# Optimization experiments

Measured on AMD Instinct MI355X. Metric: run time of the kernel, lower is better.

Reference implementation:

```python
import jax, jax.numpy as jnp
import numpy as np
import math

D_MODEL = 512
N_HEADS = 2
B, S = 2, 1024
THRESHOLD = 0.5  # kwargs default 'sparsity_threshold'


def setup_inputs() -> dict:
    key = jax.random.key(0)
    ks = jax.random.split(key, 10)
    D, H = D_MODEL, D_MODEL // 4
    std = 0.02
    return {
        "x": jax.random.normal(ks[0], (B, S, D), jnp.float32),
        "Wq": jax.random.normal(ks[1], (D, D), jnp.float32) * std,
        "Wk": jax.random.normal(ks[2], (D, D), jnp.float32) * std,
        "Wv": jax.random.normal(ks[3], (D, D), jnp.float32) * std,
        "Wo": jax.random.normal(ks[4], (D, D), jnp.float32) * std,
        "bo": jnp.zeros((D,), jnp.float32),
        "W1": jax.random.normal(ks[5], (D, H), jnp.float32) * std,
        "b1": jnp.zeros((H,), jnp.float32),
        "W2": jax.random.normal(ks[6], (H, 1), jnp.float32) * std,
        "b2": jnp.zeros((1,), jnp.float32),
    }


def reference(x, Wq, Wk, Wv, Wo, bo, W1, b1, W2, b2):
    Bsz, Seq, D = x.shape
    Hn = N_HEADS
    dh = D // Hn

    def split_heads(t):
        return t.reshape(Bsz, Seq, Hn, dh).transpose(0, 2, 1, 3)  # [B,H,S,dh]

    q = split_heads(x @ Wq)
    k = split_heads(x @ Wk)
    v = split_heads(x @ Wv)

    scores = jnp.einsum("bhid,bhjd->bhij", q, k) / math.sqrt(dh)  # [B,H,S,S]

    # head-mean features for the pairwise sparsity predictor (n_heads==2 => 2*dh == D)
    q_mean = q.mean(axis=1)  # [B,S,dh]
    k_mean = k.mean(axis=1)  # [B,S,dh]
    # Linear1 of cat([q_mean_i, k_mean_j]) splits into two halves of W1
    a = q_mean @ W1[:dh]   # [B,S,Dh4]
    c = k_mean @ W1[dh:]   # [B,S,Dh4]
    hidden = jax.nn.relu(a[:, :, None, :] + c[:, None, :, :] + b1)  # [B,S,S,Dh4]
    connection_probs = jax.nn.sigmoid(jnp.squeeze(hidden @ W2, -1) + b2[0])  # [B,S,S]

    mask = connection_probs > THRESHOLD  # [B,S,S]
    scores = jnp.where(mask[:, None, :, :], scores, jnp.float32(-1e9))
    attn = jax.nn.softmax(scores, axis=-1)  # dropout inactive in eval

    out = jnp.einsum("bhij,bhjd->bhid", attn, v)  # [B,H,S,dh]
    out = out.transpose(0, 2, 1, 3).reshape(Bsz, Seq, D)
    out = out @ Wo + bo
    return out
```

## Files before the change

### kernel.cpp

```cpp
#include <hip/hip_runtime.h>


typedef unsigned short u16t;
typedef __bf16 bf16x8 __attribute__((ext_vector_type(8)));
typedef float f32x4 __attribute__((ext_vector_type(4)));

#define B_SZ 2
#define S_SZ 1024
#define D_SZ 512
#define DH 256
#define HH 128

static __device__ __forceinline__ u16t f2b(float f) {
    unsigned int u = __builtin_bit_cast(unsigned int, f);
    u += 0x7FFFu + ((u >> 16) & 1u);
    return (u16t)(u >> 16);
}

static __device__ __forceinline__ f32x4 mfma16(bf16x8 a, bf16x8 b, f32x4 c) {
    return __builtin_amdgcn_mfma_f32_16x16x32_bf16(a, b, c, 0, 0, 0);
}

static __device__ __forceinline__ void gload16(const void* g, void* l) {
    __builtin_amdgcn_global_load_lds(
        (const __attribute__((address_space(1))) void*)g,
        (__attribute__((address_space(3))) void*)l, 16, 0, 0);
}

__global__ __launch_bounds__(256) void k_prep(
    const float* __restrict__ x,
    const float* __restrict__ Wq, const float* __restrict__ Wk,
    const float* __restrict__ Wv, const float* __restrict__ Wo,
    const float* __restrict__ W1,
    u16t* __restrict__ xb, u16t* __restrict__ WT, float* __restrict__ Beff)
{
    __shared__ float smf[1088];
    int bidx = blockIdx.x;
    int t = threadIdx.x;
    if (bidx < 1024) {
        int idx = (bidx * 256 + t) * 4;
        float4 v = *(const float4*)(x + idx);
        u16t* o = xb + idx;
        o[0] = f2b(v.x); o[1] = f2b(v.y); o[2] = f2b(v.z); o[3] = f2b(v.w);
    } else if (bidx < 2048) {
        int t2 = bidx - 1024;
        int z = t2 >> 8, rem = t2 & 255;
        int n0 = (rem & 15) * 32, k0 = (rem >> 4) * 32;
        const float* W = z == 0 ? Wq : z == 1 ? Wk : z == 2 ? Wv : Wo;
        u16t* WTz = WT + (size_t)z * D_SZ * D_SZ;
        float (*tile)[33] = (float(*)[33])smf;
        int r = t >> 3, c4 = (t & 7) * 4;
        float4 v = *(const float4*)(W + (size_t)(k0 + r) * D_SZ + n0 + c4);
        tile[r][c4] = v.x; tile[r][c4 + 1] = v.y; tile[r][c4 + 2] = v.z; tile[r][c4 + 3] = v.w;
        __syncthreads();
        u16t o[4];
        o[0] = f2b(tile[c4][r]); o[1] = f2b(tile[c4 + 1][r]);
        o[2] = f2b(tile[c4 + 2][r]); o[3] = f2b(tile[c4 + 3][r]);
        *(ushort4*)(WTz + (size_t)(n0 + r) * D_SZ + k0 + c4) = *(ushort4*)o;
    } else {
        int k = bidx - 2048;
        float* wm0 = smf;
        float* wm1 = smf + 256;
        const float* wrq = Wq + (size_t)k * D_SZ;
        const float* wrk = Wk + (size_t)k * D_SZ;
        wm0[t & 255] = 0.5f * (wrq[t & 255] + wrq[(t & 255) + DH]);
        wm1[t & 255] = 0.5f * (wrk[t & 255] + wrk[(t & 255) + DH]);
        __syncthreads();
        int half = t >> 7, hcol = t & 127;
        const float* wm = half ? wm1 : wm0;
        const float* W1h = W1 + (half ? (size_t)DH * HH : 0);
        float s = 0.f;
        for (int d = 0; d < 256; ++d) s += wm[d] * W1h[(size_t)d * HH + hcol];
        Beff[(size_t)k * 256 + half * 128 + hcol] = s;
    }
}

template<int MF, int NF>
static __device__ __forceinline__ void gemm_db(
    const u16t* __restrict__ A, int lda, const u16t* __restrict__ B, int ldb,
    int K, int tid, u16t* Als, u16t* Bls, f32x4 acc[MF][NF])
{
    const int w = tid >> 6, lane = tid & 63;
    const int lr = lane & 15, kg = lane >> 4;
    const int srow = lane >> 3;
    const int scol = ((lane & 7) ^ srow) * 8;
    const int ABUF = MF * 4096;
    const int BBUF = NF * 1024;
    auto stage = [&](int bb, int k0) {
#pragma unroll
        for (int q = 0; q < MF * 2; ++q) {
            int ci = w * (MF * 2) + q;
            gload16(A + (size_t)(ci * 8 + srow) * lda + k0 + scol,
                    Als + bb * ABUF + ci * 512);
        }
#pragma unroll
        for (int q = 0; q < NF / 2; ++q) {
            int cj = w * (NF / 2) + q;
            gload16(B + (size_t)(cj * 8 + srow) * ldb + k0 + scol,
                    Bls + bb * BBUF + cj * 512);
        }
    };
    stage(0, 0);
    __syncthreads();
    const int nt = K / 64;
    for (int t = 0; t < nt; ++t) {
        int cur = t & 1;
        if (t + 1 < nt) stage(cur ^ 1, (t + 1) * 64);
        const u16t* Ab = Als + cur * ABUF;
        const u16t* Bb = Bls + cur * BBUF;
#pragma unroll
        for (int kk = 0; kk < 2; ++kk) {
            bf16x8 af[MF], bfr[NF];
#pragma unroll
            for (int fi = 0; fi < MF; ++fi) {
                int r = w * (MF * 16) + fi * 16 + lr;
                af[fi] = *(const bf16x8*)(&Ab[r * 64 + (((kk * 4 + kg) ^ (r & 7)) << 3)]);
            }
#pragma unroll
            for (int fj = 0; fj < NF; ++fj) {
                int r = fj * 16 + lr;
                bfr[fj] = *(const bf16x8*)(&Bb[r * 64 + (((kk * 4 + kg) ^ (r & 7)) << 3)]);
            }
#pragma unroll
            for (int fi = 0; fi < MF; ++fi)
#pragma unroll
                for (int fj = 0; fj < NF; ++fj)
                    acc[fi][fj] = mfma16(af[fi], bfr[fj], acc[fi][fj]);
        }
        __syncthreads();
    }
}


__global__ __launch_bounds__(256) void k_qkvac(
    const u16t* __restrict__ xb, const u16t* __restrict__ WT,
    const float* __restrict__ x, const float* __restrict__ Beff,
    const float* __restrict__ b1,
    u16t* __restrict__ qb, u16t* __restrict__ kb, u16t* __restrict__ vT,
    float* __restrict__ a, float* __restrict__ cc)
{
    __shared__ __align__(16) char sm[49152];
    int bid = blockIdx.x;
    int t = threadIdx.x;
    if (bid < 384) {
        u16t* Als = (u16t*)sm;
        u16t* Bls = (u16t*)(sm + 32768);
        int z = bid / 128, rem = bid & 127;
        int m0 = (rem >> 3) * 128, n0 = (rem & 7) * 64;
        const u16t* A = xb + (size_t)m0 * D_SZ;
        const u16t* Bt = WT + (size_t)z * D_SZ * D_SZ + (size_t)n0 * D_SZ;
        f32x4 acc[2][4] = {};
        gemm_db<2, 4>(A, D_SZ, Bt, D_SZ, D_SZ, t, Als, Bls, acc);
        int w = t >> 6, lane = t & 63, lr = lane & 15, kg = lane >> 4;
        if (z < 2) {
            u16t (*vls)[68] = (u16t(*)[68])sm;
            float scale = z == 0 ? 0.0625f : 1.0f;
#pragma unroll
            for (int fi = 0; fi < 2; ++fi)
#pragma unroll
                for (int fj = 0; fj < 4; ++fj)
#pragma unroll
                    for (int rr = 0; rr < 4; ++rr)
                        vls[w * 32 + fi * 16 + kg * 4 + rr][fj * 16 + lr]
                            = f2b(acc[fi][fj][rr] * scale);
            __syncthreads();
            u16t* dst = z == 0 ? qb : kb;
            int c8 = (t & 7) * 8, r0 = t >> 3;
#pragma unroll
            for (int p = 0; p < 4; ++p) {
                int r = r0 + p * 32;
                *(uint4*)(dst + (size_t)(m0 + r) * D_SZ + n0 + c8) = *(const uint4*)(&vls[r][c8]);
            }
        } else {
            u16t (*vls)[136] = (u16t(*)[136])sm;
#pragma unroll
            for (int fi = 0; fi < 2; ++fi)
#pragma unroll
                for (int fj = 0; fj < 4; ++fj)
#pragma unroll
                    for (int rr = 0; rr < 4; ++rr)
                        vls[fj * 16 + lr][w * 32 + fi * 16 + kg * 4 + rr] = f2b(acc[fi][fj][rr]);
            __syncthreads();
            int b = m0 >> 10, s0 = m0 & 1023;
            int cr = t >> 2, seg = t & 3;
            const u16t* srcp = &vls[cr][seg * 32];
            u16t* dstp = vT + (((size_t)(b * D_SZ + n0 + cr)) << 10) + s0 + seg * 32;
#pragma unroll
            for (int qq = 0; qq < 4; ++qq)
                *(uint4*)(dstp + qq * 8) = *(const uint4*)(srcp + qq * 8);
        }
    } else {
        float (*xs)[68] = (float(*)[68])sm;
        float (*bsT)[68] = (float(*)[68])(sm + 17408);
        int t2 = bid - 384;
        int r0 = (t2 & 31) * 64, n0 = (t2 >> 5) * 32;
        int ti = t >> 4, tj = t & 15;
        float acc[4][2] = {};
        for (int k0 = 0; k0 < 512; k0 += 64) {
            if (k0) __syncthreads();
#pragma unroll
            for (int p = 0; p < 4; ++p) {
                int idx = t + p * 256;
                int r = idx >> 4, c4 = (idx & 15) * 4;
                *(float4*)&xs[r][c4] = *(const float4*)(x + (size_t)(r0 + r) * D_SZ + k0 + c4);
            }
#pragma unroll
            for (int p = 0; p < 2; ++p) {
                int idx = t + p * 256;
                int k = idx >> 3, n4 = (idx & 7) * 4;
                float4 v = *(const float4*)(Beff + (size_t)(k0 + k) * 256 + n0 + n4);
                bsT[n4][k] = v.x; bsT[n4 + 1][k] = v.y; bsT[n4 + 2][k] = v.z; bsT[n4 + 3][k] = v.w;
            }
            __syncthreads();
#pragma unroll
            for (int kk = 0; kk < 16; ++kk) {
                float4 xv[4], bv[2];
#pragma unroll
                for (int ri = 0; ri < 4; ++ri) xv[ri] = *(const float4*)&xs[ti + 16 * ri][kk * 4];
#pragma unroll
                for (int rj = 0; rj < 2; ++rj) bv[rj] = *(const float4*)&bsT[tj + 16 * rj][kk * 4];
#pragma unroll
                for (int ri = 0; ri < 4; ++ri)
#pragma unroll
                    for (int rj = 0; rj < 2; ++rj)
                        acc[ri][rj] += xv[ri].x * bv[rj].x + xv[ri].y * bv[rj].y
                                     + xv[ri].z * bv[rj].z + xv[ri].w * bv[rj].w;
            }
        }
        bool isA = n0 < 128;
#pragma unroll
        for (int rj = 0; rj < 2; ++rj) {
            int col = n0 + tj + 16 * rj;
            float badd = isA ? b1[col] : 0.f;
#pragma unroll
            for (int ri = 0; ri < 4; ++ri) {
                int row = r0 + ti + 16 * ri;
                if (isA) a[(size_t)row * HH + col] = acc[ri][rj] + badd;
                else     cc[(size_t)row * HH + (col - 128)] = acc[ri][rj];
            }
        }
    }
}

__global__ __launch_bounds__(256) void k_scores(
    const u16t* __restrict__ qb, const u16t* __restrict__ kb,
    const float* __restrict__ a, const float* __restrict__ c,
    const float* __restrict__ W2, const float* __restrict__ b2,
    u16t* __restrict__ P, float* __restrict__ lpart)
{
    __shared__ __align__(16) char sm[55296];
    float (*at)[132] = (float(*)[132])sm;
    float (*ct)[132] = (float(*)[132])(sm + 33792);
    unsigned char (*msk)[64] = (unsigned char(*)[64])(sm + 50688);
    float* w2s = (float*)(sm + 54784);
    int b = blockIdx.z, mt = blockIdx.y, jb = blockIdx.x;
    int m0 = mt * 64, j0 = jb * 64;
    int t = threadIdx.x;
    if (t < 128) w2s[t] = W2[t];
#pragma unroll
    for (int p = 0; p < 8; ++p) {
        int idx = t + p * 256;
        int r = idx >> 5, c4 = (idx & 31) * 4;
        *(float4*)&at[r][c4] = *(const float4*)(a + ((size_t)(b * S_SZ + m0 + r)) * HH + c4);
    }
    float fb2 = b2[0];
    int ti = t >> 4, tj = t & 15;
#pragma unroll
    for (int jh = 0; jh < 2; ++jh) {
        __syncthreads();
#pragma unroll
        for (int p = 0; p < 4; ++p) {
            int idx = t + p * 256;
            int r = idx >> 5, c4 = (idx & 31) * 4;
            *(float4*)&ct[r][c4] =
                *(const float4*)(c + ((size_t)(b * S_SZ + j0 + jh * 32 + r)) * HH + c4);
        }
        __syncthreads();
        float accm[4][2];
#pragma unroll
        for (int ri = 0; ri < 4; ++ri)
#pragma unroll
            for (int rj = 0; rj < 2; ++rj) accm[ri][rj] = fb2;
#pragma unroll 2
        for (int h4 = 0; h4 < 32; ++h4) {
            float4 wv = ((const float4*)w2s)[h4];
            float4 av[4], cv[2];
#pragma unroll
            for (int ri = 0; ri < 4; ++ri) av[ri] = *(const float4*)&at[ti + 16 * ri][h4 * 4];
#pragma unroll
            for (int rj = 0; rj < 2; ++rj) cv[rj] = *(const float4*)&ct[tj + 16 * rj][h4 * 4];
#pragma unroll
            for (int ri = 0; ri < 4; ++ri)
#pragma unroll
                for (int rj = 0; rj < 2; ++rj) {
                    accm[ri][rj] += fmaxf(av[ri].x + cv[rj].x, 0.f) * wv.x;
                    accm[ri][rj] += fmaxf(av[ri].y + cv[rj].y, 0.f) * wv.y;
                    accm[ri][rj] += fmaxf(av[ri].z + cv[rj].z, 0.f) * wv.z;
                    accm[ri][rj] += fmaxf(av[ri].w + cv[rj].w, 0.f) * wv.w;
                }
        }
#pragma unroll
        for (int ri = 0; ri < 4; ++ri)
#pragma unroll
            for (int rj = 0; rj < 2; ++rj)
                msk[ti + 16 * ri][jh * 32 + tj + 16 * rj] = accm[ri][rj] > 0.f ? 1 : 0;
    }
    __syncthreads();
    u16t* Als = (u16t*)sm;
    u16t* Bls = (u16t*)(sm + 16384);
    const u16t* A = qb + (size_t)(b * S_SZ + m0) * D_SZ;
    const u16t* B = kb + (size_t)(b * S_SZ + j0) * D_SZ;
    const int w = t >> 6, lane = t & 63, lr = lane & 15, kg = lane >> 4;
    const int srow = lane >> 3;
    const int scol = ((lane & 7) ^ srow) * 8;
    auto stage = [&](int bb, int k0) {
#pragma unroll
        for (int q = 0; q < 2; ++q) {
            int ci = w * 2 + q;
            gload16(A + (size_t)(ci * 8 + srow) * D_SZ + k0 + scol, Als + bb * 4096 + ci * 512);
            gload16(B + (size_t)(ci * 8 + srow) * D_SZ + k0 + scol, Bls + bb * 4096 + ci * 512);
        }
    };
    f32x4 acc0[4] = {}, acc1[4] = {};
    stage(0, 0);
    __syncthreads();
#pragma unroll
    for (int t8 = 0; t8 < 8; ++t8) {
        int cur = t8 & 1;
        if (t8 < 7) stage(cur ^ 1, (t8 + 1) * 64);
        const u16t* Ab = Als + cur * 4096;
        const u16t* Bb = Bls + cur * 4096;
#pragma unroll
        for (int kk = 0; kk < 2; ++kk) {
            int ra = w * 16 + lr;
            bf16x8 af = *(const bf16x8*)(&Ab[ra * 64 + (((kk * 4 + kg) ^ (ra & 7)) << 3)]);
            bf16x8 bfr[4];
#pragma unroll
            for (int fj = 0; fj < 4; ++fj) {
                int rb = fj * 16 + lr;
                bfr[fj] = *(const bf16x8*)(&Bb[rb * 64 + (((kk * 4 + kg) ^ (rb & 7)) << 3)]);
            }
            if (t8 < 4) {
#pragma unroll
                for (int fj = 0; fj < 4; ++fj) acc0[fj] = mfma16(af, bfr[fj], acc0[fj]);
            } else {
#pragma unroll
                for (int fj = 0; fj < 4; ++fj) acc1[fj] = mfma16(af, bfr[fj], acc1[fj]);
            }
        }
        __syncthreads();
    }
    u16t (*vls)[68] = (u16t(*)[68])sm;
#pragma unroll
    for (int h = 0; h < 2; ++h) {
#pragma unroll
        for (int rr = 0; rr < 4; ++rr) {
            int il = w * 16 + kg * 4 + rr;
            float rs = 0.f;
#pragma unroll
            for (int fj = 0; fj < 4; ++fj) {
                int jl = fj * 16 + lr;
                float s = h ? acc1[fj][rr] : acc0[fj][rr];
                float e = msk[il][jl] ? __expf(s) : 0.f;
                if (h) acc1[fj][rr] = e; else acc0[fj][rr] = e;
                rs += e;
            }
            rs += __shfl_xor(rs, 1); rs += __shfl_xor(rs, 2);
            rs += __shfl_xor(rs, 4); rs += __shfl_xor(rs, 8);
            if (lr == 0)
                lpart[((size_t)(jb * 4 + b * 2 + h) << 10) + m0 + il] = rs;
        }
#pragma unroll
        for (int fj = 0; fj < 4; ++fj)
#pragma unroll
            for (int rr = 0; rr < 4; ++rr)
                vls[w * 16 + kg * 4 + rr][fj * 16 + lr]
                    = f2b(h ? acc1[fj][rr] : acc0[fj][rr]);
        __syncthreads();
        int r = t >> 2, c16 = (t & 3) * 16;
        u16t* dstp = P + ((size_t)(b * 2 + h) << 20) + ((size_t)(m0 + r) << 10) + j0 + c16;
        *(uint4*)dstp = *(const uint4*)(&vls[r][c16]);
        *(uint4*)(dstp + 8) = *(const uint4*)(&vls[r][c16 + 8]);
        __syncthreads();
    }
}

__global__ __launch_bounds__(256) void k_pv(
    const u16t* __restrict__ P, const u16t* __restrict__ vT,
    const float* __restrict__ lpart, u16t* __restrict__ ao)
{
    __shared__ __align__(16) u16t sm[12288];
    __shared__ float invl[64];
    u16t* Als = sm;
    u16t* Bls = sm + 8192;
    int bh = blockIdx.z, b = bh >> 1, h = bh & 1;
    int m0 = blockIdx.y * 64, n0 = blockIdx.x * 32;
    int t = threadIdx.x;
    if (t < 64) {
        float l = 0.f;
        for (int jb = 0; jb < 16; ++jb)
            l += lpart[((size_t)(jb * 4 + bh) << 10) + m0 + t];
        invl[t] = l > 0.f ? 1.0f / l : 0.f;
    }
    const u16t* A = P + ((size_t)bh << 20) + (size_t)m0 * S_SZ;
    const u16t* Bt = vT + ((size_t)(b * D_SZ + h * DH + n0)) * S_SZ;
    f32x4 acc[1][2] = {};
    gemm_db<1, 2>(A, S_SZ, Bt, S_SZ, S_SZ, t, Als, Bls, acc);
    int w = t >> 6, lane = t & 63, lr = lane & 15, kg = lane >> 4;
    u16t (*ols)[40] = (u16t(*)[40])sm;
#pragma unroll
    for (int fj = 0; fj < 2; ++fj)
#pragma unroll
        for (int rr = 0; rr < 4; ++rr) {
            int rl = w * 16 + kg * 4 + rr;
            ols[rl][fj * 16 + lr] = f2b(acc[0][fj][rr] * invl[rl]);
        }
    __syncthreads();
    int r = t >> 2, c8 = (t & 3) * 8;
    *(uint4*)(ao + ((size_t)(b * S_SZ + m0 + r)) * D_SZ + h * DH + n0 + c8)
        = *(const uint4*)(&ols[r][c8]);
}

__global__ __launch_bounds__(256) void k_out(
    const u16t* __restrict__ ao, const u16t* __restrict__ WoT,
    const float* __restrict__ bo, float* __restrict__ out)
{
    __shared__ __align__(16) u16t sm[12288];
    u16t* Als = sm;
    u16t* Bls = sm + 8192;
    int m0 = blockIdx.y * 64, n0 = blockIdx.x * 32;
    const u16t* A = ao + (size_t)m0 * D_SZ;
    const u16t* Bt = WoT + (size_t)n0 * D_SZ;
    f32x4 acc[1][2] = {};
    gemm_db<1, 2>(A, D_SZ, Bt, D_SZ, D_SZ, threadIdx.x, Als, Bls, acc);
    int w = threadIdx.x >> 6, lane = threadIdx.x & 63, lr = lane & 15, kg = lane >> 4;
    float (*ols)[36] = (float(*)[36])sm;
#pragma unroll
    for (int fj = 0; fj < 2; ++fj)
#pragma unroll
        for (int rr = 0; rr < 4; ++rr) {
            int rl = w * 16 + kg * 4 + rr;
            ols[rl][fj * 16 + lr] = acc[0][fj][rr] + bo[n0 + fj * 16 + lr];
        }
    __syncthreads();
    int r0 = threadIdx.x >> 3, c4 = (threadIdx.x & 7) * 4;
#pragma unroll
    for (int p = 0; p < 2; ++p) {
        int r = r0 + p * 32;
        *(float4*)(out + (size_t)(m0 + r) * D_SZ + n0 + c4) = *(const float4*)(&ols[r][c4]);
    }
}

extern "C" void kernel_launch(void* const* d_in, const int* in_sizes, int n_in,
                              void* d_out, int out_size, void* d_ws, size_t ws_size,
                              hipStream_t stream)
{
    const float* x  = (const float*)d_in[0];
    const float* Wq = (const float*)d_in[1];
    const float* Wk = (const float*)d_in[2];
    const float* Wv = (const float*)d_in[3];
    const float* Wo = (const float*)d_in[4];
    const float* bo = (const float*)d_in[5];
    const float* W1 = (const float*)d_in[6];
    const float* b1 = (const float*)d_in[7];
    const float* W2 = (const float*)d_in[8];
    const float* b2 = (const float*)d_in[9];
    float* out = (float*)d_out;

    char* ws = (char*)d_ws;
    size_t off = 0;
    auto carve = [&](size_t bytes) { void* p = ws + off; off += (bytes + 255) & ~(size_t)255; return p; };
    u16t* xb   = (u16t*)carve((size_t)2048 * 512 * 2);
    u16t* WT   = (u16t*)carve((size_t)4 * 512 * 512 * 2);
    u16t* qb   = (u16t*)carve((size_t)2048 * 512 * 2);
    u16t* kb   = (u16t*)carve((size_t)2048 * 512 * 2);
    u16t* vT   = (u16t*)carve((size_t)2 * 512 * 1024 * 2);
    float* Beff = (float*)carve((size_t)512 * 256 * 4);
    float* a   = (float*)carve((size_t)2048 * 128 * 4);
    float* c   = (float*)carve((size_t)2048 * 128 * 4);
    u16t* P    = (u16t*)carve((size_t)4 * 1024 * 1024 * 2);
    float* lpart = (float*)carve((size_t)16 * 4 * 1024 * 4);
    u16t* ao   = (u16t*)carve((size_t)2048 * 512 * 2);
    (void)ws_size;

    k_prep<<<dim3(2560), dim3(256), 0, stream>>>(x, Wq, Wk, Wv, Wo, W1, xb, WT, Beff);
    k_qkvac<<<dim3(640), dim3(256), 0, stream>>>(xb, WT, x, Beff, b1, qb, kb, vT, a, c);
    k_scores<<<dim3(16, 16, 2), dim3(256), 0, stream>>>(qb, kb, a, c, W2, b2, P, lpart);
    k_pv<<<dim3(8, 16, 4), dim3(256), 0, stream>>>(P, vT, lpart, ao);
    k_out<<<dim3(16, 32), dim3(256), 0, stream>>>(ao, WT + (size_t)3 * 512 * 512, bo, out);
}
```

Measured before the change: 100.3 us.

## Halve k_scores row tile to 32 and remap waves to column strips

Halves the query-row tile of the scores/mask kernel from 64 to 32 rows, doubling the grid to 1024 blocks and shrinking shared memory so more blocks fit per CU. Each wave now owns a 16-column strip of keys instead of a 16-row strip, so row sums are reduced across waves through a small shared buffer before being written. The aim is more parallelism and occupancy on the many-CU GPU, at the cost of reloading the key tile and c-vectors twice as often and an extra barrier for the cross-wave sum.

New measurement: 99.78 us (median of 2 runs). Within noise of the previous version (-0.5%).

```diff
diff --git a/kernel.cpp b/kernel.cpp
--- a/kernel.cpp
+++ b/kernel.cpp
@@ -248,23 +248,24 @@
     const float* __restrict__ W2, const float* __restrict__ b2,
     u16t* __restrict__ P, float* __restrict__ lpart)
 {
-    __shared__ __align__(16) char sm[55296];
+    __shared__ __align__(16) char sm[36864];
     float (*at)[132] = (float(*)[132])sm;
-    float (*ct)[132] = (float(*)[132])(sm + 33792);
-    unsigned char (*msk)[64] = (unsigned char(*)[64])(sm + 50688);
-    float* w2s = (float*)(sm + 54784);
+    float (*ct)[132] = (float(*)[132])(sm + 16896);
+    unsigned char (*msk)[64] = (unsigned char(*)[64])(sm + 33792);
+    float* w2s  = (float*)(sm + 35840);
+    float* lsum = (float*)(sm + 36352);
     int b = blockIdx.z, mt = blockIdx.y, jb = blockIdx.x;
-    int m0 = mt * 64, j0 = jb * 64;
+    int m0 = mt * 32, j0 = jb * 64;
     int t = threadIdx.x;
     if (t < 128) w2s[t] = W2[t];
-#pragma unroll
-    for (int p = 0; p < 8; ++p) {
+    float fb2 = b2[0];
+    int ti = t >> 4, tj = t & 15;
+#pragma unroll
+    for (int p = 0; p < 4; ++p) {
         int idx = t + p * 256;
         int r = idx >> 5, c4 = (idx & 31) * 4;
         *(float4*)&at[r][c4] = *(const float4*)(a + ((size_t)(b * S_SZ + m0 + r)) * HH + c4);
     }
-    float fb2 = b2[0];
-    int ti = t >> 4, tj = t & 15;
 #pragma unroll
     for (int jh = 0; jh < 2; ++jh) {
         __syncthreads();
@@ -276,21 +277,21 @@
                 *(const float4*)(c + ((size_t)(b * S_SZ + j0 + jh * 32 + r)) * HH + c4);
         }
         __syncthreads();
-        float accm[4][2];
-#pragma unroll
-        for (int ri = 0; ri < 4; ++ri)
+        float accm[2][2];
+#pragma unroll
+        for (int ri = 0; ri < 2; ++ri)
 #pragma unroll
             for (int rj = 0; rj < 2; ++rj) accm[ri][rj] = fb2;
 #pragma unroll 2
         for (int h4 = 0; h4 < 32; ++h4) {
             float4 wv = ((const float4*)w2s)[h4];
-            float4 av[4], cv[2];
-#pragma unroll
-            for (int ri = 0; ri < 4; ++ri) av[ri] = *(const float4*)&at[ti + 16 * ri][h4 * 4];
+            float4 av[2], cv[2];
+#pragma unroll
+            for (int ri = 0; ri < 2; ++ri) av[ri] = *(const float4*)&at[ti + 16 * ri][h4 * 4];
 #pragma unroll
             for (int rj = 0; rj < 2; ++rj) cv[rj] = *(const float4*)&ct[tj + 16 * rj][h4 * 4];
 #pragma unroll
-            for (int ri = 0; ri < 4; ++ri)
+            for (int ri = 0; ri < 2; ++ri)
 #pragma unroll
                 for (int rj = 0; rj < 2; ++rj) {
                     accm[ri][rj] += fmaxf(av[ri].x + cv[rj].x, 0.f) * wv.x;
@@ -300,52 +301,52 @@
                 }
         }
 #pragma unroll
-        for (int ri = 0; ri < 4; ++ri)
+        for (int ri = 0; ri < 2; ++ri)
 #pragma unroll
             for (int rj = 0; rj < 2; ++rj)
                 msk[ti + 16 * ri][jh * 32 + tj + 16 * rj] = accm[ri][rj] > 0.f ? 1 : 0;
     }
     __syncthreads();
     u16t* Als = (u16t*)sm;
-    u16t* Bls = (u16t*)(sm + 16384);
+    u16t* Bls = (u16t*)(sm + 8192);
     const u16t* A = qb + (size_t)(b * S_SZ + m0) * D_SZ;
     const u16t* B = kb + (size_t)(b * S_SZ + j0) * D_SZ;
     const int w = t >> 6, lane = t & 63, lr = lane & 15, kg = lane >> 4;
     const int srow = lane >> 3;
     const int scol = ((lane & 7) ^ srow) * 8;
     auto stage = [&](int bb, int k0) {
+        gload16(A + (size_t)(w * 8 + srow) * D_SZ + k0 + scol, Als + bb * 2048 + w * 512);
 #pragma unroll
         for (int q = 0; q < 2; ++q) {
-            int ci = w * 2 + q;
-            gload16(A + (size_t)(ci * 8 + srow) * D_SZ + k0 + scol, Als + bb * 4096 + ci * 512);
-            gload16(B + (size_t)(ci * 8 + srow) * D_SZ + k0 + scol, Bls + bb * 4096 + ci * 512);
+            int cj = w * 2 + q;
+            gload16(B + (size_t)(cj * 8 + srow) * D_SZ + k0 + scol, Bls + bb * 4096 + cj * 512);
         }
     };
-    f32x4 acc0[4] = {}, acc1[4] = {};
+    f32x4 acc0[2] = {}, acc1[2] = {};
     stage(0, 0);
     __syncthreads();
 #pragma unroll
     for (int t8 = 0; t8 < 8; ++t8) {
         int cur = t8 & 1;
         if (t8 < 7) stage(cur ^ 1, (t8 + 1) * 64);
-        const u16t* Ab = Als + cur * 4096;
+        const u16t* Ab = Als + cur * 2048;
         const u16t* Bb = Bls + cur * 4096;
 #pragma unroll
         for (int kk = 0; kk < 2; ++kk) {
-            int ra = w * 16 + lr;
-            bf16x8 af = *(const bf16x8*)(&Ab[ra * 64 + (((kk * 4 + kg) ^ (ra & 7)) << 3)]);
-            bf16x8 bfr[4];
-#pragma unroll
-            for (int fj = 0; fj < 4; ++fj) {
-                int rb = fj * 16 + lr;
-                bfr[fj] = *(const bf16x8*)(&Bb[rb * 64 + (((kk * 4 + kg) ^ (rb & 7)) << 3)]);
+            int rb = w * 16 + lr;
+            bf16x8 bfr = *(const bf16x8*)(&Bb[rb * 64 + (((kk * 4 + kg) ^ (rb & 7)) << 3)]);
+            bf16x8 af[2];
+#pragma unroll
+            for (int fi = 0; fi < 2; ++fi) {
+                int ra = fi * 16 + lr;
+                af[fi] = *(const bf16x8*)(&Ab[ra * 64 + (((kk * 4 + kg) ^ (ra & 7)) << 3)]);
             }
             if (t8 < 4) {
 #pragma unroll
-                for (int fj = 0; fj < 4; ++fj) acc0[fj] = mfma16(af, bfr[fj], acc0[fj]);
+                for (int fi = 0; fi < 2; ++fi) acc0[fi] = mfma16(af[fi], bfr, acc0[fi]);
             } else {
 #pragma unroll
-                for (int fj = 0; fj < 4; ++fj) acc1[fj] = mfma16(af, bfr[fj], acc1[fj]);
+                for (int fi = 0; fi < 2; ++fi) acc1[fi] = mfma16(af[fi], bfr, acc1[fi]);
             }
         }
         __syncthreads();
@@ -354,33 +355,39 @@
 #pragma unroll
     for (int h = 0; h < 2; ++h) {
 #pragma unroll
-        for (int rr = 0; rr < 4; ++rr) {
-            int il = w * 16 + kg * 4 + rr;
-            float rs = 0.f;
-#pragma unroll
-            for (int fj = 0; fj < 4; ++fj) {
-                int jl = fj * 16 + lr;
-                float s = h ? acc1[fj][rr] : acc0[fj][rr];
+        for (int fi = 0; fi < 2; ++fi)
+#pragma unroll
+            for (int rr = 0; rr < 4; ++rr) {
+                int il = fi * 16 + kg * 4 + rr;
+                int jl = w * 16 + lr;
+                float s = h ? acc1[fi][rr] : acc0[fi][rr];
                 float e = msk[il][jl] ? __expf(s) : 0.f;
-                if (h) acc1[fj][rr] = e; else acc0[fj][rr] = e;
-                rs += e;
-            }
-            rs += __shfl_xor(rs, 1); rs += __shfl_xor(rs, 2);
-            rs += __shfl_xor(rs, 4); rs += __shfl_xor(rs, 8);
-            if (lr == 0)
-                lpart[((size_t)(jb * 4 + b * 2 + h) << 10) + m0 + il] = rs;
-        }
-#pragma unroll
-        for (int fj = 0; fj < 4; ++fj)
+                if (h) acc1[fi][rr] = e; else acc0[fi][rr] = e;
+            }
+#pragma unroll
+        for (int fi = 0; fi < 2; ++fi)
+#pragma unroll
+            for (int rr = 0; rr < 4; ++rr) {
+                float rs = h ? acc1[fi][rr] : acc0[fi][rr];
+                rs += __shfl_xor(rs, 1); rs += __shfl_xor(rs, 2);
+                rs += __shfl_xor(rs, 4); rs += __shfl_xor(rs, 8);
+                if (lr == 0) lsum[w * 32 + fi * 16 + kg * 4 + rr] = rs;
+            }
+        __syncthreads();
+        if (t < 32) {
+            float l = lsum[t] + lsum[32 + t] + lsum[64 + t] + lsum[96 + t];
+            lpart[((size_t)(jb * 4 + b * 2 + h) << 10) + m0 + t] = l;
+        }
+#pragma unroll
+        for (int fi = 0; fi < 2; ++fi)
 #pragma unroll
             for (int rr = 0; rr < 4; ++rr)
-                vls[w * 16 + kg * 4 + rr][fj * 16 + lr]
-                    = f2b(h ? acc1[fj][rr] : acc0[fj][rr]);
-        __syncthreads();
-        int r = t >> 2, c16 = (t & 3) * 16;
-        u16t* dstp = P + ((size_t)(b * 2 + h) << 20) + ((size_t)(m0 + r) << 10) + j0 + c16;
-        *(uint4*)dstp = *(const uint4*)(&vls[r][c16]);
-        *(uint4*)(dstp + 8) = *(const uint4*)(&vls[r][c16 + 8]);
+                vls[fi * 16 + kg * 4 + rr][w * 16 + lr]
+                    = f2b(h ? acc1[fi][rr] : acc0[fi][rr]);
+        __syncthreads();
+        int r = t >> 3, c8 = (t & 7) * 8;
+        *(uint4*)(P + ((size_t)(b * 2 + h) << 20) + ((size_t)(m0 + r) << 10) + j0 + c8)
+            = *(const uint4*)(&vls[r][c8]);
         __syncthreads();
     }
 }
@@ -485,7 +492,7 @@
 
     k_prep<<<dim3(2560), dim3(256), 0, stream>>>(x, Wq, Wk, Wv, Wo, W1, xb, WT, Beff);
     k_qkvac<<<dim3(640), dim3(256), 0, stream>>>(xb, WT, x, Beff, b1, qb, kb, vT, a, c);
-    k_scores<<<dim3(16, 16, 2), dim3(256), 0, stream>>>(qb, kb, a, c, W2, b2, P, lpart);
+    k_scores<<<dim3(16, 32, 2), dim3(256), 0, stream>>>(qb, kb, a, c, W2, b2, P, lpart);
     k_pv<<<dim3(8, 16, 4), dim3(256), 0, stream>>>(P, vT, lpart, ao);
     k_out<<<dim3(16, 32), dim3(256), 0, stream>>>(ao, WT + (size_t)3 * 512 * 512, bo, out);
 }
```
